# Performance work log

Measured on AMD Instinct MI355X. Metric: run time of the kernel, lower is better.

Reference implementation:

```python
import jax, jax.numpy as jnp
import numpy as np

N_NODES = 100000
N_EDGES = 1600000
NUM_GRAPHS = 64
IN_CH = 128
OUT_CH = 10


def setup_inputs() -> dict:
    key = jax.random.key(0)
    ks = jax.random.split(key, 12)
    s = 0.05
    x = jax.random.normal(ks[0], (N_NODES, IN_CH), dtype=jnp.float32)
    edge_index = jax.random.randint(ks[1], (2, N_EDGES), 0, N_NODES, dtype=jnp.int64)
    batch = jnp.sort(jax.random.randint(ks[2], (N_NODES,), 0, NUM_GRAPHS, dtype=jnp.int64))
    return {
        "x": x,
        "edge_index": edge_index,
        "batch": batch,
        "W1": jax.random.normal(ks[3], (IN_CH, 64), dtype=jnp.float32) * s,
        "b1": jnp.zeros((64,), dtype=jnp.float32),
        "W2": jax.random.normal(ks[4], (64, 64), dtype=jnp.float32) * s,
        "b2": jnp.zeros((64,), dtype=jnp.float32),
        "W3": jax.random.normal(ks[5], (64, 64), dtype=jnp.float32) * s,
        "b3": jnp.zeros((64,), dtype=jnp.float32),
        "W4": jax.random.normal(ks[6], (64, 128), dtype=jnp.float32) * s,
        "b4": jnp.zeros((128,), dtype=jnp.float32),
        "Wfc": jax.random.normal(ks[7], (128, OUT_CH), dtype=jnp.float32) * s,
        "bfc": jnp.zeros((OUT_CH,), dtype=jnp.float32),
    }


def _gin_agg(x, edge_index):
    # PyG GINConv (eps=0): h_i = x_i + sum_{j->i} x_j
    src, dst = edge_index[0], edge_index[1]
    agg = jax.ops.segment_sum(x[src], dst, num_segments=N_NODES)
    return x + agg


def reference(x, edge_index, batch, W1, b1, W2, b2, W3, b3, W4, b4, Wfc, bfc):
    # conv1: GINConv(Linear(in,64) -> ReLU -> Linear(64,64)), then outer ReLU
    h = _gin_agg(x, edge_index)
    h = jax.nn.relu(h @ W1 + b1) @ W2 + b2
    h = jax.nn.relu(h)
    # dropout is identity at eval time
    # conv2: GINConv(Linear(64,64) -> ReLU -> Linear(64,128))
    h = _gin_agg(h, edge_index)
    h = jax.nn.relu(h @ W3 + b3) @ W4 + b4
    # global mean pool over graphs
    sums = jax.ops.segment_sum(h, batch, num_segments=NUM_GRAPHS)
    counts = jax.ops.segment_sum(jnp.ones((N_NODES,), dtype=h.dtype), batch, num_segments=NUM_GRAPHS)
    pooled = sums / jnp.maximum(counts, 1.0)[:, None]
    logits = pooled @ Wfc + bfc
    return jax.nn.log_softmax(logits, axis=1)
```

## Files before the change

### kernel.cpp

```cpp
#include <hip/hip_runtime.h>
#include <cmath>

#define N_NODES    100000
#define N_EDGES    1600000
#define NUM_GRAPHS 64

#define BUCK_W     512
#define NBUCK      196
#define EPB        2048
#define NB1        782
#define GEMM_GS    782
#define AGG_NPB    64

typedef __attribute__((ext_vector_type(8))) short bf16x8;
typedef __attribute__((ext_vector_type(4))) float f32x4;

__device__ __forceinline__ ushort f2bf(float x) {
    union { float f; uint u; } v; v.f = x;
    uint r = v.u + 0x7fffu + ((v.u >> 16) & 1u);
    return (ushort)(r >> 16);
}
__device__ __forceinline__ float bf2f(ushort u) {
    union { uint u; float f; } v; v.u = ((uint)u) << 16;
    return v.f;
}

__global__ __launch_bounds__(256) void k1_hist_gemm(
    const int* __restrict__ dst, int* __restrict__ bcount,
    const float* __restrict__ x, const float* __restrict__ W1,
    ushort* __restrict__ y)
{
    if (blockIdx.x < NB1) {
        __shared__ int shist[NBUCK];
        int tid = threadIdx.x;
        for (int i = tid; i < NBUCK; i += 256) shist[i] = 0;
        __syncthreads();
        int e0 = blockIdx.x * EPB + tid;
        #pragma unroll
        for (int k = 0; k < EPB / 256; ++k) {
            int e = e0 + k * 256;
            if (e < N_EDGES) atomicAdd(&shist[dst[e] >> 9], 1);
        }
        __syncthreads();
        for (int i = tid; i < NBUCK; i += 256)
            bcount[blockIdx.x * NBUCK + i] = shist[i];
        return;
    }
    int bid = blockIdx.x - NB1;
    int lane = threadIdx.x & 63, wave = threadIdx.x >> 6;
    int lg = lane >> 4, lm = lane & 15;

    bf16x8 Bf[4][4];
    #pragma unroll
    for (int kc = 0; kc < 4; ++kc)
        #pragma unroll
        for (int cb = 0; cb < 4; ++cb) {
            bf16x8 t;
            #pragma unroll
            for (int i = 0; i < 8; ++i)
                t[i] = (short)f2bf(W1[(kc * 32 + lg * 8 + i) * 64 + cb * 16 + lm]);
            Bf[kc][cb] = t;
        }

    const int ntiles = N_NODES / 16;
    for (int tile = bid * 4 + wave; tile < ntiles; tile += GEMM_GS * 4) {
        int r = tile * 16 + lm;
        f32x4 acc[4] = {};
        #pragma unroll
        for (int kc = 0; kc < 4; ++kc) {
            const float* p = x + (size_t)r * 128 + kc * 32 + lg * 8;
            float4 a0 = *(const float4*)p;
            float4 a1 = *(const float4*)(p + 4);
            bf16x8 af;
            af[0] = (short)f2bf(a0.x); af[1] = (short)f2bf(a0.y);
            af[2] = (short)f2bf(a0.z); af[3] = (short)f2bf(a0.w);
            af[4] = (short)f2bf(a1.x); af[5] = (short)f2bf(a1.y);
            af[6] = (short)f2bf(a1.z); af[7] = (short)f2bf(a1.w);
            #pragma unroll
            for (int cb = 0; cb < 4; ++cb)
                acc[cb] = __builtin_amdgcn_mfma_f32_16x16x32_bf16(af, Bf[kc][cb], acc[cb], 0, 0, 0);
        }
        #pragma unroll
        for (int cb = 0; cb < 4; ++cb)
            #pragma unroll
            for (int i = 0; i < 4; ++i)
                y[(size_t)(tile * 16 + lg * 4 + i) * 64 + cb * 16 + lm] = f2bf(acc[cb][i]);
    }
}

#define SCH 4
__global__ __launch_bounds__(256) void p2a_scan(
    const int* __restrict__ bcount, int* __restrict__ basetab,
    int* __restrict__ btot)
{
    __shared__ int sh[256];
    int b = blockIdx.x, tid = threadIdx.x;
    int v[SCH];
    int tsum = 0;
    #pragma unroll
    for (int j = 0; j < SCH; ++j) {
        int blk = tid * SCH + j;
        v[j] = (blk < NB1) ? bcount[(size_t)blk * NBUCK + b] : 0;
        tsum += v[j];
    }
    sh[tid] = tsum;
    __syncthreads();
    for (int off = 1; off < 256; off <<= 1) {
        int t = (tid >= off) ? sh[tid - off] : 0;
        __syncthreads();
        sh[tid] += t;
        __syncthreads();
    }
    if (tid == 255) btot[b] = sh[255];
    int excl = sh[tid] - tsum;
    #pragma unroll
    for (int j = 0; j < SCH; ++j) {
        int blk = tid * SCH + j;
        if (blk < NB1) basetab[(size_t)b * NB1 + blk] = excl;
        excl += v[j];
    }
}

__global__ __launch_bounds__(256) void p2b_scan(
    const int* __restrict__ btot, int* __restrict__ gbase,
    float* __restrict__ pooled)
{
    int tid = threadIdx.x;
    for (int i = tid; i < NUM_GRAPHS * 128; i += 256) pooled[i] = 0.0f;
    __shared__ int v[NBUCK];
    for (int j = tid; j < NBUCK; j += 256) v[j] = btot[j];
    __syncthreads();
    if (tid == 0) {
        int run = 0;
        for (int j = 0; j < NBUCK; ++j) { int t = v[j]; v[j] = run; run += t; }
        gbase[NBUCK] = run;
    }
    __syncthreads();
    for (int j = tid; j < NBUCK; j += 256) gbase[j] = v[j];
}

__global__ __launch_bounds__(256) void p3_partition(
    const int* __restrict__ src, const int* __restrict__ dst,
    const int* __restrict__ basetab, const int* __restrict__ gbase,
    uint* __restrict__ epack)
{
    __shared__ int cur[NBUCK];
    int blk = blockIdx.x, tid = threadIdx.x;
    for (int i = tid; i < NBUCK; i += 256)
        cur[i] = basetab[(size_t)i * NB1 + blk] + gbase[i];
    __syncthreads();
    int e0 = blk * EPB + tid;
    #pragma unroll
    for (int k = 0; k < EPB / 256; ++k) {
        int e = e0 + k * 256;
        if (e < N_EDGES) {
            int d = dst[e], s = src[e];
            int bin = d >> 9;
            int pos = atomicAdd(&cur[bin], 1);
            epack[pos] = ((uint)(d & 511) << 17) | (uint)s;
        }
    }
}

__global__ __launch_bounds__(256) void p4_fine(
    const uint* __restrict__ epack, const int* __restrict__ gbase,
    int* __restrict__ rowptr, int* __restrict__ esrc)
{
    __shared__ int hist[BUCK_W];
    int b = blockIdx.x, tid = threadIdx.x;
    int beg = gbase[b], end = gbase[b + 1];
    for (int i = tid; i < BUCK_W; i += 256) hist[i] = 0;
    __syncthreads();
    for (int e = beg + tid; e < end; e += 256)
        atomicAdd(&hist[epack[e] >> 17], 1);
    __syncthreads();
    if (tid == 0) {
        int run = 0;
        for (int i = 0; i < BUCK_W; ++i) { int t = hist[i]; hist[i] = run; run += t; }
    }
    __syncthreads();
    for (int i = tid; i < BUCK_W; i += 256) {
        int n = b * BUCK_W + i;
        if (n < N_NODES) rowptr[n] = beg + hist[i];
    }
    if (b == NBUCK - 1 && tid == 0) rowptr[N_NODES] = end;
    __syncthreads();
    for (int e = beg + tid; e < end; e += 256) {
        uint v = epack[e];
        int slot = beg + atomicAdd(&hist[v >> 17], 1);
        esrc[slot] = (int)(v & 0x1FFFFu);
    }
}

__global__ __launch_bounds__(256) void agg_bf16_v4(
    const uint4* __restrict__ in4, uint4* __restrict__ out4,
    const int* __restrict__ rowptr, const int* __restrict__ esrc)
{
    __shared__ int pool;
    if (threadIdx.x == 0) pool = 0;
    __syncthreads();

    int sub = threadIdx.x & 7;
    int wl  = threadIdx.x & 63;
    int base = blockIdx.x * AGG_NPB;
    int nmax = min(AGG_NPB, N_NODES - base);

    for (;;) {
        int n = 0;
        if (sub == 0) n = atomicAdd(&pool, 1);
        n = __shfl(n, wl & 56, 64);
        if (n >= nmax) break;
        int node = base + n;

        float a[8] = {0, 0, 0, 0, 0, 0, 0, 0};

#define ACCUM(V) do {                                                   \
        uint _w[4] = {(V).x, (V).y, (V).z, (V).w};                      \
        _Pragma("unroll")                                               \
        for (int j = 0; j < 4; ++j) {                                   \
            a[2 * j]     += bf2f((ushort)(_w[j] & 0xffffu));            \
            a[2 * j + 1] += bf2f((ushort)(_w[j] >> 16));                \
        }                                                               \
    } while (0)

        {
            uint4 v = in4[(size_t)node * 8 + sub];
            ACCUM(v);
        }
        int e = rowptr[node], end = rowptr[node + 1];
        for (; e + 8 <= end; e += 8) {
            int i0 = esrc[e],     i1 = esrc[e + 1], i2 = esrc[e + 2], i3 = esrc[e + 3];
            int i4 = esrc[e + 4], i5 = esrc[e + 5], i6 = esrc[e + 6], i7 = esrc[e + 7];
            uint4 v0 = in4[(size_t)i0 * 8 + sub];
            uint4 v1 = in4[(size_t)i1 * 8 + sub];
            uint4 v2 = in4[(size_t)i2 * 8 + sub];
            uint4 v3 = in4[(size_t)i3 * 8 + sub];
            uint4 v4 = in4[(size_t)i4 * 8 + sub];
            uint4 v5 = in4[(size_t)i5 * 8 + sub];
            uint4 v6 = in4[(size_t)i6 * 8 + sub];
            uint4 v7 = in4[(size_t)i7 * 8 + sub];
            ACCUM(v0); ACCUM(v1); ACCUM(v2); ACCUM(v3);
            ACCUM(v4); ACCUM(v5); ACCUM(v6); ACCUM(v7);
        }
        if (e + 4 <= end) {
            int i0 = esrc[e], i1 = esrc[e + 1], i2 = esrc[e + 2], i3 = esrc[e + 3];
            uint4 v0 = in4[(size_t)i0 * 8 + sub];
            uint4 v1 = in4[(size_t)i1 * 8 + sub];
            uint4 v2 = in4[(size_t)i2 * 8 + sub];
            uint4 v3 = in4[(size_t)i3 * 8 + sub];
            ACCUM(v0); ACCUM(v1); ACCUM(v2); ACCUM(v3);
            e += 4;
        }
        for (; e < end; ++e) {
            uint4 v = in4[(size_t)esrc[e] * 8 + sub];
            ACCUM(v);
        }
#undef ACCUM

        uint4 o;
        o.x = (uint)f2bf(a[0]) | ((uint)f2bf(a[1]) << 16);
        o.y = (uint)f2bf(a[2]) | ((uint)f2bf(a[3]) << 16);
        o.z = (uint)f2bf(a[4]) | ((uint)f2bf(a[5]) << 16);
        o.w = (uint)f2bf(a[6]) | ((uint)f2bf(a[7]) << 16);
        out4[(size_t)node * 8 + sub] = o;
    }
}

__global__ __launch_bounds__(256) void fused_mid(
    const ushort* __restrict__ yagg, const float* __restrict__ b1,
    const float* __restrict__ W2, const float* __restrict__ b2,
    const float* __restrict__ W3, ushort* __restrict__ z)
{
    __shared__ __align__(16) float trs[4][16 * 68];
    int lane = threadIdx.x & 63, wave = threadIdx.x >> 6;
    int lg = lane >> 4, lm = lane & 15;

    bf16x8 B2[2][4], B3[2][4];
    #pragma unroll
    for (int kc = 0; kc < 2; ++kc)
        #pragma unroll
        for (int cb = 0; cb < 4; ++cb) {
            bf16x8 t2, t3;
            #pragma unroll
            for (int i = 0; i < 8; ++i) {
                int k = kc * 32 + lg * 8 + i;
                int cc = cb * 16 + lm;
                t2[i] = (short)f2bf(W2[k * 64 + cc]);
                t3[i] = (short)f2bf(W3[k * 64 + cc]);
            }
            B2[kc][cb] = t2; B3[kc][cb] = t3;
        }
    float b1r[2][8];
    #pragma unroll
    for (int kc = 0; kc < 2; ++kc)
        #pragma unroll
        for (int i = 0; i < 8; ++i)
            b1r[kc][i] = b1[kc * 32 + lg * 8 + i];
    float b2r[4];
    #pragma unroll
    for (int cb = 0; cb < 4; ++cb) b2r[cb] = b2[cb * 16 + lm];

    const int ntiles = N_NODES / 16;
    for (int tile = blockIdx.x * 4 + wave; tile < ntiles; tile += GEMM_GS * 4) {
        int r = tile * 16 + lm;
        bf16x8 A1[2];
        #pragma unroll
        for (int kc = 0; kc < 2; ++kc) {
            uint4 raw = *(const uint4*)(yagg + (size_t)r * 64 + kc * 32 + lg * 8);
            uint w[4] = {raw.x, raw.y, raw.z, raw.w};
            bf16x8 t;
            #pragma unroll
            for (int j = 0; j < 4; ++j) {
                float flo = bf2f((ushort)(w[j] & 0xffffu)) + b1r[kc][2 * j];
                float fhi = bf2f((ushort)(w[j] >> 16)) + b1r[kc][2 * j + 1];
                t[2 * j]     = (short)f2bf(fmaxf(flo, 0.0f));
                t[2 * j + 1] = (short)f2bf(fmaxf(fhi, 0.0f));
            }
            A1[kc] = t;
        }
        f32x4 acc[4] = {};
        #pragma unroll
        for (int kc = 0; kc < 2; ++kc)
            #pragma unroll
            for (int cb = 0; cb < 4; ++cb)
                acc[cb] = __builtin_amdgcn_mfma_f32_16x16x32_bf16(A1[kc], B2[kc][cb], acc[cb], 0, 0, 0);
        #pragma unroll
        for (int cb = 0; cb < 4; ++cb)
            #pragma unroll
            for (int i = 0; i < 4; ++i)
                trs[wave][(lg * 4 + i) * 68 + cb * 16 + lm] = fmaxf(acc[cb][i] + b2r[cb], 0.0f);
        bf16x8 A2[2];
        #pragma unroll
        for (int kc = 0; kc < 2; ++kc) {
            const float* p = &trs[wave][lm * 68 + kc * 32 + lg * 8];
            float4 u0 = *(const float4*)p;
            float4 u1 = *(const float4*)(p + 4);
            bf16x8 t;
            t[0] = (short)f2bf(u0.x); t[1] = (short)f2bf(u0.y);
            t[2] = (short)f2bf(u0.z); t[3] = (short)f2bf(u0.w);
            t[4] = (short)f2bf(u1.x); t[5] = (short)f2bf(u1.y);
            t[6] = (short)f2bf(u1.z); t[7] = (short)f2bf(u1.w);
            A2[kc] = t;
        }
        f32x4 acc2[4] = {};
        #pragma unroll
        for (int kc = 0; kc < 2; ++kc)
            #pragma unroll
            for (int cb = 0; cb < 4; ++cb)
                acc2[cb] = __builtin_amdgcn_mfma_f32_16x16x32_bf16(A2[kc], B3[kc][cb], acc2[cb], 0, 0, 0);
        #pragma unroll
        for (int cb = 0; cb < 4; ++cb)
            #pragma unroll
            for (int i = 0; i < 4; ++i)
                z[(size_t)(tile * 16 + lg * 4 + i) * 64 + cb * 16 + lm] = f2bf(acc2[cb][i]);
    }
}

__global__ __launch_bounds__(256) void k4_mfma_pool(
    const ushort* __restrict__ zagg, const float* __restrict__ b3,
    const float* __restrict__ W4, const float* __restrict__ b4,
    const int* __restrict__ batch, float* __restrict__ pooled)
{
    int lane = threadIdx.x & 63, wave = threadIdx.x >> 6;
    int lg = lane >> 4, lm = lane & 15;

    bf16x8 B4[2][8];
    #pragma unroll
    for (int kc = 0; kc < 2; ++kc)
        #pragma unroll
        for (int cb = 0; cb < 8; ++cb) {
            bf16x8 t;
            #pragma unroll
            for (int i = 0; i < 8; ++i)
                t[i] = (short)f2bf(W4[(kc * 32 + lg * 8 + i) * 128 + cb * 16 + lm]);
            B4[kc][cb] = t;
        }
    float b3r[2][8];
    #pragma unroll
    for (int kc = 0; kc < 2; ++kc)
        #pragma unroll
        for (int i = 0; i < 8; ++i)
            b3r[kc][i] = b3[kc * 32 + lg * 8 + i];
    float b4r[8];
    #pragma unroll
    for (int cb = 0; cb < 8; ++cb) b4r[cb] = b4[cb * 16 + lm];

    const int NT = N_NODES / 16;
    const int TPW = 4;
    int w = blockIdx.x * 4 + wave;
    int t0 = w * TPW;
    if (t0 >= NT) return;
    int t1 = min(t0 + TPW, NT);

    float pacc[8] = {0, 0, 0, 0, 0, 0, 0, 0};
    int curg = batch[t0 * 16];

#define FLUSH(G) do {                                                     \
        _Pragma("unroll")                                                 \
        for (int cb = 0; cb < 8; ++cb) {                                  \
            float v = pacc[cb];                                           \
            v += __shfl_xor(v, 16, 64);                                   \
            v += __shfl_xor(v, 32, 64);                                   \
            if (lane < 16) unsafeAtomicAdd(&pooled[(G) * 128 + cb * 16 + lm], v); \
            pacc[cb] = 0.0f;                                              \
        }                                                                 \
    } while (0)

    for (int t = t0; t < t1; ++t) {
        int rbase = t * 16;
        int r = rbase + lm;
        bf16x8 A[2];
        #pragma unroll
        for (int kc = 0; kc < 2; ++kc) {
            uint4 raw = *(const uint4*)(zagg + (size_t)r * 64 + kc * 32 + lg * 8);
            uint wv[4] = {raw.x, raw.y, raw.z, raw.w};
            bf16x8 tt;
            #pragma unroll
            for (int j = 0; j < 4; ++j) {
                float flo = bf2f((ushort)(wv[j] & 0xffffu)) + b3r[kc][2 * j];
                float fhi = bf2f((ushort)(wv[j] >> 16))    + b3r[kc][2 * j + 1];
                tt[2 * j]     = (short)f2bf(fmaxf(flo, 0.0f));
                tt[2 * j + 1] = (short)f2bf(fmaxf(fhi, 0.0f));
            }
            A[kc] = tt;
        }
        f32x4 acc[8] = {};
        #pragma unroll
        for (int kc = 0; kc < 2; ++kc)
            #pragma unroll
            for (int cb = 0; cb < 8; ++cb)
                acc[cb] = __builtin_amdgcn_mfma_f32_16x16x32_bf16(A[kc], B4[kc][cb], acc[cb], 0, 0, 0);

        int g0 = batch[rbase], g15 = batch[rbase + 15];
        if (g0 != curg) { FLUSH(curg); curg = g0; }
        if (g0 == g15) {
            #pragma unroll
            for (int cb = 0; cb < 8; ++cb)
                pacc[cb] += acc[cb][0] + acc[cb][1] + acc[cb][2] + acc[cb][3]
                            + 4.0f * b4r[cb];
        } else {
            FLUSH(curg);
            #pragma unroll
            for (int i = 0; i < 4; ++i) {
                int gi = batch[rbase + lg * 4 + i];
                #pragma unroll
                for (int cb = 0; cb < 8; ++cb)
                    unsafeAtomicAdd(&pooled[gi * 128 + cb * 16 + lm],
                                    acc[cb][i] + b4r[cb]);
            }
            curg = g15;
        }
    }
    FLUSH(curg);
#undef FLUSH
}

__global__ void head_kernel(
    const float* __restrict__ pooled, const int* __restrict__ batch,
    const float* __restrict__ Wfc, const float* __restrict__ bfc,
    float* __restrict__ out)
{
    int g = threadIdx.x;
    if (g >= NUM_GRAPHS) return;

    int lo = 0, hi = N_NODES;
    while (lo < hi) { int mid = (lo + hi) >> 1; if (batch[mid] < g) lo = mid + 1; else hi = mid; }
    int beg = lo;
    lo = 0; hi = N_NODES;
    while (lo < hi) { int mid = (lo + hi) >> 1; if (batch[mid] < g + 1) lo = mid + 1; else hi = mid; }
    int cnt = lo - beg;
    float inv = 1.0f / fmaxf((float)cnt, 1.0f);

    float logits[10];
    for (int o = 0; o < 10; ++o) {
        float acc = 0.0f;
        for (int k = 0; k < 128; ++k)
            acc = fmaf(pooled[g * 128 + k], Wfc[k * 10 + o], acc);
        logits[o] = acc * inv + bfc[o];
    }
    float m = -INFINITY;
    for (int o = 0; o < 10; ++o) m = fmaxf(m, logits[o]);
    float s = 0.0f;
    for (int o = 0; o < 10; ++o) s += expf(logits[o] - m);
    float ls = logf(s);
    for (int o = 0; o < 10; ++o) out[g * 10 + o] = logits[o] - m - ls;
}

extern "C" void kernel_launch(void* const* d_in, const int* in_sizes, int n_in,
                              void* d_out, int out_size, void* d_ws, size_t ws_size,
                              hipStream_t stream)
{
    const float* x     = (const float*)d_in[0];
    const int*   ei    = (const int*)d_in[1];
    const int*   src   = ei;
    const int*   dst   = ei + N_EDGES;
    const int*   batch = (const int*)d_in[2];
    const float* W1  = (const float*)d_in[3];
    const float* b1  = (const float*)d_in[4];
    const float* W2  = (const float*)d_in[5];
    const float* b2  = (const float*)d_in[6];
    const float* W3  = (const float*)d_in[7];
    const float* b3  = (const float*)d_in[8];
    const float* W4  = (const float*)d_in[9];
    const float* b4  = (const float*)d_in[10];
    const float* Wfc = (const float*)d_in[11];
    const float* bfc = (const float*)d_in[12];
    float* out = (float*)d_out;

    char* ws = (char*)d_ws;
    ushort* bufA   = (ushort*)(ws);
    ushort* bufB   = (ushort*)(ws + 12800000);
    int*  esrc     = (int*) (ws + 25600000);
    uint* epack    = (uint*)(ws + 32000000);
    int*  rowptr   = (int*) (ws + 38400000);
    int*  bcount   = (int*) (ws + 38800016);
    int*  basetab  = (int*) (ws + 39413120);
    int*  btot     = (int*) (ws + 40026224);
    int*  gbase    = (int*) (ws + 40027008);
    float* pooled  = (float*)(ws + 40027808);

    k1_hist_gemm<<<NB1 + GEMM_GS, 256, 0, stream>>>(dst, bcount, x, W1, bufA);
    p2a_scan<<<NBUCK, 256, 0, stream>>>(bcount, basetab, btot);
    p2b_scan<<<1, 256, 0, stream>>>(btot, gbase, pooled);
    p3_partition<<<NB1, 256, 0, stream>>>(src, dst, basetab, gbase, epack);
    p4_fine<<<NBUCK, 256, 0, stream>>>(epack, gbase, rowptr, esrc);

    agg_bf16_v4<<<(N_NODES + AGG_NPB - 1) / AGG_NPB, 256, 0, stream>>>(
        (const uint4*)bufA, (uint4*)bufB, rowptr, esrc);
    fused_mid<<<GEMM_GS, 256, 0, stream>>>(bufB, b1, W2, b2, W3, bufA);

    agg_bf16_v4<<<(N_NODES + AGG_NPB - 1) / AGG_NPB, 256, 0, stream>>>(
        (const uint4*)bufA, (uint4*)bufB, rowptr, esrc);
    {
        const int NT = N_NODES / 16;
        const int TPW = 4;
        int blocks = (NT + 4 * TPW - 1) / (4 * TPW);
        k4_mfma_pool<<<blocks, 256, 0, stream>>>(bufB, b3, W4, b4, batch, pooled);
    }

    head_kernel<<<1, 64, 0, stream>>>(pooled, batch, Wfc, bfc, out);
}
```

Before: 199.4 us.

## Fuse neighbor aggregation into following MFMA GEMM kernels via swizzled shared memory

Merges each bf16 gather-aggregation kernel with the dense MLP kernel that follows it. Each block aggregates 256 nodes, applies bias and ReLU, and stores the rows in XOR-swizzled LDS, which its waves then read as MFMA operands. This removes two launches and the global write and re-read of the aggregated intermediate. The cost is a large LDS footprint per block, which lowers occupancy for the latency-bound gather, plus a barrier between the gather and GEMM phases. The GEMM grid is now fixed at one 256-node tile per block.

Result: slower. 246.5 us (+23.6%).

```diff
diff --git a/kernel.cpp b/kernel.cpp
--- a/kernel.cpp
+++ b/kernel.cpp
@@ -10,7 +10,8 @@
 #define EPB        2048
 #define NB1        782
 #define GEMM_GS    782
-#define AGG_NPB    64
+#define FUSE_NPB   256
+#define NFUSE      ((N_NODES + FUSE_NPB - 1) / FUSE_NPB)
 
 typedef __attribute__((ext_vector_type(8))) short bf16x8;
 typedef __attribute__((ext_vector_type(4))) float f32x4;
@@ -23,6 +24,59 @@
 __device__ __forceinline__ float bf2f(ushort u) {
     union { uint u; float f; } v; v.u = ((uint)u) << 16;
     return v.f;
+}
+
+__device__ __forceinline__ void accum8(float* a, uint4 V) {
+    uint w[4] = {V.x, V.y, V.z, V.w};
+    #pragma unroll
+    for (int j = 0; j < 4; ++j) {
+        a[2 * j]     += bf2f((ushort)(w[j] & 0xffffu));
+        a[2 * j + 1] += bf2f((ushort)(w[j] >> 16));
+    }
+}
+
+__device__ __forceinline__ void gather_node(
+    const uint4* __restrict__ in4, const int* __restrict__ rowptr,
+    const int* __restrict__ esrc, int node, int sub, float a[8])
+{
+    #pragma unroll
+    for (int j = 0; j < 8; ++j) a[j] = 0.0f;
+    accum8(a, in4[(size_t)node * 8 + sub]);
+    int e = rowptr[node], end = rowptr[node + 1];
+    for (; e + 8 <= end; e += 8) {
+        int i0 = esrc[e],     i1 = esrc[e + 1], i2 = esrc[e + 2], i3 = esrc[e + 3];
+        int i4 = esrc[e + 4], i5 = esrc[e + 5], i6 = esrc[e + 6], i7 = esrc[e + 7];
+        uint4 v0 = in4[(size_t)i0 * 8 + sub];
+        uint4 v1 = in4[(size_t)i1 * 8 + sub];
+        uint4 v2 = in4[(size_t)i2 * 8 + sub];
+        uint4 v3 = in4[(size_t)i3 * 8 + sub];
+        uint4 v4 = in4[(size_t)i4 * 8 + sub];
+        uint4 v5 = in4[(size_t)i5 * 8 + sub];
+        uint4 v6 = in4[(size_t)i6 * 8 + sub];
+        uint4 v7 = in4[(size_t)i7 * 8 + sub];
+        accum8(a, v0); accum8(a, v1); accum8(a, v2); accum8(a, v3);
+        accum8(a, v4); accum8(a, v5); accum8(a, v6); accum8(a, v7);
+    }
+    if (e + 4 <= end) {
+        int i0 = esrc[e], i1 = esrc[e + 1], i2 = esrc[e + 2], i3 = esrc[e + 3];
+        uint4 v0 = in4[(size_t)i0 * 8 + sub];
+        uint4 v1 = in4[(size_t)i1 * 8 + sub];
+        uint4 v2 = in4[(size_t)i2 * 8 + sub];
+        uint4 v3 = in4[(size_t)i3 * 8 + sub];
+        accum8(a, v0); accum8(a, v1); accum8(a, v2); accum8(a, v3);
+        e += 4;
+    }
+    for (; e < end; ++e)
+        accum8(a, in4[(size_t)esrc[e] * 8 + sub]);
+}
+
+__device__ __forceinline__ uint4 pack_relu(const float a[8], const float bg[8]) {
+    uint4 o;
+    o.x = (uint)f2bf(fmaxf(a[0] + bg[0], 0.0f)) | ((uint)f2bf(fmaxf(a[1] + bg[1], 0.0f)) << 16);
+    o.y = (uint)f2bf(fmaxf(a[2] + bg[2], 0.0f)) | ((uint)f2bf(fmaxf(a[3] + bg[3], 0.0f)) << 16);
+    o.z = (uint)f2bf(fmaxf(a[4] + bg[4], 0.0f)) | ((uint)f2bf(fmaxf(a[5] + bg[5], 0.0f)) << 16);
+    o.w = (uint)f2bf(fmaxf(a[6] + bg[6], 0.0f)) | ((uint)f2bf(fmaxf(a[7] + bg[7], 0.0f)) << 16);
+    return o;
 }
 
 __global__ __launch_bounds__(256) void k1_hist_gemm(
@@ -192,90 +246,23 @@
     }
 }
 
-__global__ __launch_bounds__(256) void agg_bf16_v4(
-    const uint4* __restrict__ in4, uint4* __restrict__ out4,
-    const int* __restrict__ rowptr, const int* __restrict__ esrc)
-{
-    __shared__ int pool;
-    if (threadIdx.x == 0) pool = 0;
-    __syncthreads();
-
-    int sub = threadIdx.x & 7;
-    int wl  = threadIdx.x & 63;
-    int base = blockIdx.x * AGG_NPB;
-    int nmax = min(AGG_NPB, N_NODES - base);
-
-    for (;;) {
-        int n = 0;
-        if (sub == 0) n = atomicAdd(&pool, 1);
-        n = __shfl(n, wl & 56, 64);
-        if (n >= nmax) break;
-        int node = base + n;
-
-        float a[8] = {0, 0, 0, 0, 0, 0, 0, 0};
-
-#define ACCUM(V) do {                                                   \
-        uint _w[4] = {(V).x, (V).y, (V).z, (V).w};                      \
-        _Pragma("unroll")                                               \
-        for (int j = 0; j < 4; ++j) {                                   \
-            a[2 * j]     += bf2f((ushort)(_w[j] & 0xffffu));            \
-            a[2 * j + 1] += bf2f((ushort)(_w[j] >> 16));                \
-        }                                                               \
-    } while (0)
-
-        {
-            uint4 v = in4[(size_t)node * 8 + sub];
-            ACCUM(v);
-        }
-        int e = rowptr[node], end = rowptr[node + 1];
-        for (; e + 8 <= end; e += 8) {
-            int i0 = esrc[e],     i1 = esrc[e + 1], i2 = esrc[e + 2], i3 = esrc[e + 3];
-            int i4 = esrc[e + 4], i5 = esrc[e + 5], i6 = esrc[e + 6], i7 = esrc[e + 7];
-            uint4 v0 = in4[(size_t)i0 * 8 + sub];
-            uint4 v1 = in4[(size_t)i1 * 8 + sub];
-            uint4 v2 = in4[(size_t)i2 * 8 + sub];
-            uint4 v3 = in4[(size_t)i3 * 8 + sub];
-            uint4 v4 = in4[(size_t)i4 * 8 + sub];
-            uint4 v5 = in4[(size_t)i5 * 8 + sub];
-            uint4 v6 = in4[(size_t)i6 * 8 + sub];
-            uint4 v7 = in4[(size_t)i7 * 8 + sub];
-            ACCUM(v0); ACCUM(v1); ACCUM(v2); ACCUM(v3);
-            ACCUM(v4); ACCUM(v5); ACCUM(v6); ACCUM(v7);
-        }
-        if (e + 4 <= end) {
-            int i0 = esrc[e], i1 = esrc[e + 1], i2 = esrc[e + 2], i3 = esrc[e + 3];
-            uint4 v0 = in4[(size_t)i0 * 8 + sub];
-            uint4 v1 = in4[(size_t)i1 * 8 + sub];
-            uint4 v2 = in4[(size_t)i2 * 8 + sub];
-            uint4 v3 = in4[(size_t)i3 * 8 + sub];
-            ACCUM(v0); ACCUM(v1); ACCUM(v2); ACCUM(v3);
-            e += 4;
-        }
-        for (; e < end; ++e) {
-            uint4 v = in4[(size_t)esrc[e] * 8 + sub];
-            ACCUM(v);
-        }
-#undef ACCUM
-
-        uint4 o;
-        o.x = (uint)f2bf(a[0]) | ((uint)f2bf(a[1]) << 16);
-        o.y = (uint)f2bf(a[2]) | ((uint)f2bf(a[3]) << 16);
-        o.z = (uint)f2bf(a[4]) | ((uint)f2bf(a[5]) << 16);
-        o.w = (uint)f2bf(a[6]) | ((uint)f2bf(a[7]) << 16);
-        out4[(size_t)node * 8 + sub] = o;
-    }
-}
-
-__global__ __launch_bounds__(256) void fused_mid(
-    const ushort* __restrict__ yagg, const float* __restrict__ b1,
+__global__ __launch_bounds__(256) void fused_agg_mid(
+    const uint4* __restrict__ in4, const int* __restrict__ rowptr,
+    const int* __restrict__ esrc, const float* __restrict__ b1,
     const float* __restrict__ W2, const float* __restrict__ b2,
     const float* __restrict__ W3, ushort* __restrict__ z)
 {
+    __shared__ uint4 srow4[FUSE_NPB * 8];
     __shared__ __align__(16) float trs[4][16 * 68];
-    int lane = threadIdx.x & 63, wave = threadIdx.x >> 6;
+    __shared__ int pool;
+
+    int tid = threadIdx.x;
+    if (tid == 0) pool = 0;
+    int lane = tid & 63, wave = tid >> 6;
     int lg = lane >> 4, lm = lane & 15;
-
-    bf16x8 B2[2][4], B3[2][4];
+    int sub = tid & 7;
+
+    bf16x8 B2f[2][4], B3f[2][4];
     #pragma unroll
     for (int kc = 0; kc < 2; ++kc)
         #pragma unroll
@@ -288,42 +275,48 @@
                 t2[i] = (short)f2bf(W2[k * 64 + cc]);
                 t3[i] = (short)f2bf(W3[k * 64 + cc]);
             }
-            B2[kc][cb] = t2; B3[kc][cb] = t3;
-        }
-    float b1r[2][8];
-    #pragma unroll
-    for (int kc = 0; kc < 2; ++kc)
-        #pragma unroll
-        for (int i = 0; i < 8; ++i)
-            b1r[kc][i] = b1[kc * 32 + lg * 8 + i];
+            B2f[kc][cb] = t2; B3f[kc][cb] = t3;
+        }
     float b2r[4];
     #pragma unroll
     for (int cb = 0; cb < 4; ++cb) b2r[cb] = b2[cb * 16 + lm];
-
-    const int ntiles = N_NODES / 16;
-    for (int tile = blockIdx.x * 4 + wave; tile < ntiles; tile += GEMM_GS * 4) {
-        int r = tile * 16 + lm;
+    float bg[8];
+    #pragma unroll
+    for (int j = 0; j < 8; ++j) bg[j] = b1[sub * 8 + j];
+
+    __syncthreads();
+
+    int base = blockIdx.x * FUSE_NPB;
+    int nmax = min(FUSE_NPB, N_NODES - base);
+
+    for (;;) {
+        int n = 0;
+        if (sub == 0) n = atomicAdd(&pool, 1);
+        n = __shfl(n, lane & 56, 64);
+        if (n >= nmax) break;
+        float a[8];
+        gather_node(in4, rowptr, esrc, base + n, sub, a);
+        srow4[n * 8 + (sub ^ (n & 7))] = pack_relu(a, bg);
+    }
+    __syncthreads();
+
+    #pragma unroll
+    for (int t = 0; t < 4; ++t) {
+        int lr0 = wave * 64 + t * 16;
+        int gr0 = base + lr0;
+        if (gr0 >= N_NODES) break;
+        int lr = lr0 + lm;
         bf16x8 A1[2];
         #pragma unroll
-        for (int kc = 0; kc < 2; ++kc) {
-            uint4 raw = *(const uint4*)(yagg + (size_t)r * 64 + kc * 32 + lg * 8);
-            uint w[4] = {raw.x, raw.y, raw.z, raw.w};
-            bf16x8 t;
-            #pragma unroll
-            for (int j = 0; j < 4; ++j) {
-                float flo = bf2f((ushort)(w[j] & 0xffffu)) + b1r[kc][2 * j];
-                float fhi = bf2f((ushort)(w[j] >> 16)) + b1r[kc][2 * j + 1];
-                t[2 * j]     = (short)f2bf(fmaxf(flo, 0.0f));
-                t[2 * j + 1] = (short)f2bf(fmaxf(fhi, 0.0f));
-            }
-            A1[kc] = t;
-        }
+        for (int kc = 0; kc < 2; ++kc)
+            A1[kc] = *reinterpret_cast<const bf16x8*>(
+                &srow4[lr * 8 + ((4 * kc + lg) ^ (lm & 7))]);
         f32x4 acc[4] = {};
         #pragma unroll
         for (int kc = 0; kc < 2; ++kc)
             #pragma unroll
             for (int cb = 0; cb < 4; ++cb)
-                acc[cb] = __builtin_amdgcn_mfma_f32_16x16x32_bf16(A1[kc], B2[kc][cb], acc[cb], 0, 0, 0);
+                acc[cb] = __builtin_amdgcn_mfma_f32_16x16x32_bf16(A1[kc], B2f[kc][cb], acc[cb], 0, 0, 0);
         #pragma unroll
         for (int cb = 0; cb < 4; ++cb)
             #pragma unroll
@@ -335,36 +328,43 @@
             const float* p = &trs[wave][lm * 68 + kc * 32 + lg * 8];
             float4 u0 = *(const float4*)p;
             float4 u1 = *(const float4*)(p + 4);
-            bf16x8 t;
-            t[0] = (short)f2bf(u0.x); t[1] = (short)f2bf(u0.y);
-            t[2] = (short)f2bf(u0.z); t[3] = (short)f2bf(u0.w);
-            t[4] = (short)f2bf(u1.x); t[5] = (short)f2bf(u1.y);
-            t[6] = (short)f2bf(u1.z); t[7] = (short)f2bf(u1.w);
-            A2[kc] = t;
+            bf16x8 tt;
+            tt[0] = (short)f2bf(u0.x); tt[1] = (short)f2bf(u0.y);
+            tt[2] = (short)f2bf(u0.z); tt[3] = (short)f2bf(u0.w);
+            tt[4] = (short)f2bf(u1.x); tt[5] = (short)f2bf(u1.y);
+            tt[6] = (short)f2bf(u1.z); tt[7] = (short)f2bf(u1.w);
+            A2[kc] = tt;
         }
         f32x4 acc2[4] = {};
         #pragma unroll
         for (int kc = 0; kc < 2; ++kc)
             #pragma unroll
             for (int cb = 0; cb < 4; ++cb)
-                acc2[cb] = __builtin_amdgcn_mfma_f32_16x16x32_bf16(A2[kc], B3[kc][cb], acc2[cb], 0, 0, 0);
+                acc2[cb] = __builtin_amdgcn_mfma_f32_16x16x32_bf16(A2[kc], B3f[kc][cb], acc2[cb], 0, 0, 0);
         #pragma unroll
         for (int cb = 0; cb < 4; ++cb)
             #pragma unroll
             for (int i = 0; i < 4; ++i)
-                z[(size_t)(tile * 16 + lg * 4 + i) * 64 + cb * 16 + lm] = f2bf(acc2[cb][i]);
-    }
-}
-
-__global__ __launch_bounds__(256) void k4_mfma_pool(
-    const ushort* __restrict__ zagg, const float* __restrict__ b3,
+                z[(size_t)(gr0 + lg * 4 + i) * 64 + cb * 16 + lm] = f2bf(acc2[cb][i]);
+    }
+}
+
+__global__ __launch_bounds__(256) void fused_agg_k4(
+    const uint4* __restrict__ in4, const int* __restrict__ rowptr,
+    const int* __restrict__ esrc, const float* __restrict__ b3,
     const float* __restrict__ W4, const float* __restrict__ b4,
     const int* __restrict__ batch, float* __restrict__ pooled)
 {
-    int lane = threadIdx.x & 63, wave = threadIdx.x >> 6;
+    __shared__ uint4 srow4[FUSE_NPB * 8];
+    __shared__ int pool;
+
+    int tid = threadIdx.x;
+    if (tid == 0) pool = 0;
+    int lane = tid & 63, wave = tid >> 6;
     int lg = lane >> 4, lm = lane & 15;
-
-    bf16x8 B4[2][8];
+    int sub = tid & 7;
+
+    bf16x8 B4f[2][8];
     #pragma unroll
     for (int kc = 0; kc < 2; ++kc)
         #pragma unroll
@@ -373,27 +373,35 @@
             #pragma unroll
             for (int i = 0; i < 8; ++i)
                 t[i] = (short)f2bf(W4[(kc * 32 + lg * 8 + i) * 128 + cb * 16 + lm]);
-            B4[kc][cb] = t;
-        }
-    float b3r[2][8];
-    #pragma unroll
-    for (int kc = 0; kc < 2; ++kc)
-        #pragma unroll
-        for (int i = 0; i < 8; ++i)
-            b3r[kc][i] = b3[kc * 32 + lg * 8 + i];
+            B4f[kc][cb] = t;
+        }
     float b4r[8];
     #pragma unroll
     for (int cb = 0; cb < 8; ++cb) b4r[cb] = b4[cb * 16 + lm];
-
-    const int NT = N_NODES / 16;
-    const int TPW = 4;
-    int w = blockIdx.x * 4 + wave;
-    int t0 = w * TPW;
-    if (t0 >= NT) return;
-    int t1 = min(t0 + TPW, NT);
-
+    float bg[8];
+    #pragma unroll
+    for (int j = 0; j < 8; ++j) bg[j] = b3[sub * 8 + j];
+
+    __syncthreads();
+
+    int base = blockIdx.x * FUSE_NPB;
+    int nmax = min(FUSE_NPB, N_NODES - base);
+
+    for (;;) {
+        int n = 0;
+        if (sub == 0) n = atomicAdd(&pool, 1);
+        n = __shfl(n, lane & 56, 64);
+        if (n >= nmax) break;
+        float a[8];
+        gather_node(in4, rowptr, esrc, base + n, sub, a);
+        srow4[n * 8 + (sub ^ (n & 7))] = pack_relu(a, bg);
+    }
+    __syncthreads();
+
+    int gr_w = base + wave * 64;
+    if (gr_w >= N_NODES) return;
     float pacc[8] = {0, 0, 0, 0, 0, 0, 0, 0};
-    int curg = batch[t0 * 16];
+    int curg = batch[gr_w];
 
 #define FLUSH(G) do {                                                     \
         _Pragma("unroll")                                                 \
@@ -406,30 +414,23 @@
         }                                                                 \
     } while (0)
 
-    for (int t = t0; t < t1; ++t) {
-        int rbase = t * 16;
-        int r = rbase + lm;
+    #pragma unroll
+    for (int t = 0; t < 4; ++t) {
+        int lr0 = wave * 64 + t * 16;
+        int rbase = base + lr0;
+        if (rbase >= N_NODES) break;
+        int lr = lr0 + lm;
         bf16x8 A[2];
         #pragma unroll
-        for (int kc = 0; kc < 2; ++kc) {
-            uint4 raw = *(const uint4*)(zagg + (size_t)r * 64 + kc * 32 + lg * 8);
-            uint wv[4] = {raw.x, raw.y, raw.z, raw.w};
-            bf16x8 tt;
-            #pragma unroll
-            for (int j = 0; j < 4; ++j) {
-                float flo = bf2f((ushort)(wv[j] & 0xffffu)) + b3r[kc][2 * j];
-                float fhi = bf2f((ushort)(wv[j] >> 16))    + b3r[kc][2 * j + 1];
-                tt[2 * j]     = (short)f2bf(fmaxf(flo, 0.0f));
-                tt[2 * j + 1] = (short)f2bf(fmaxf(fhi, 0.0f));
-            }
-            A[kc] = tt;
-        }
+        for (int kc = 0; kc < 2; ++kc)
+            A[kc] = *reinterpret_cast<const bf16x8*>(
+                &srow4[lr * 8 + ((4 * kc + lg) ^ (lm & 7))]);
         f32x4 acc[8] = {};
         #pragma unroll
         for (int kc = 0; kc < 2; ++kc)
             #pragma unroll
             for (int cb = 0; cb < 8; ++cb)
-                acc[cb] = __builtin_amdgcn_mfma_f32_16x16x32_bf16(A[kc], B4[kc][cb], acc[cb], 0, 0, 0);
+                acc[cb] = __builtin_amdgcn_mfma_f32_16x16x32_bf16(A[kc], B4f[kc][cb], acc[cb], 0, 0, 0);
 
         int g0 = batch[rbase], g15 = batch[rbase + 15];
         if (g0 != curg) { FLUSH(curg); curg = g0; }
@@ -525,18 +526,11 @@
     p3_partition<<<NB1, 256, 0, stream>>>(src, dst, basetab, gbase, epack);
     p4_fine<<<NBUCK, 256, 0, stream>>>(epack, gbase, rowptr, esrc);
 
-    agg_bf16_v4<<<(N_NODES + AGG_NPB - 1) / AGG_NPB, 256, 0, stream>>>(
-        (const uint4*)bufA, (uint4*)bufB, rowptr, esrc);
-    fused_mid<<<GEMM_GS, 256, 0, stream>>>(bufB, b1, W2, b2, W3, bufA);
-
-    agg_bf16_v4<<<(N_NODES + AGG_NPB - 1) / AGG_NPB, 256, 0, stream>>>(
-        (const uint4*)bufA, (uint4*)bufB, rowptr, esrc);
-    {
-        const int NT = N_NODES / 16;
-        const int TPW = 4;
-        int blocks = (NT + 4 * TPW - 1) / (4 * TPW);
-        k4_mfma_pool<<<blocks, 256, 0, stream>>>(bufB, b3, W4, b4, batch, pooled);
-    }
+    fused_agg_mid<<<NFUSE, 256, 0, stream>>>(
+        (const uint4*)bufA, rowptr, esrc, b1, W2, b2, W3, bufB);
+
+    fused_agg_k4<<<NFUSE, 256, 0, stream>>>(
+        (const uint4*)bufB, rowptr, esrc, b3, W4, b4, batch, pooled);
 
     head_kernel<<<1, 64, 0, stream>>>(pooled, batch, Wfc, bfc, out);
 }
```
